# Performance work log

Hardware: AMD Instinct MI355X
Metric: run time of the kernel (lower is better)

The kernel has to match this reference:

```python
import jax, jax.numpy as jnp
import numpy as np

N_NODES = 50000
N_EDGES = 500000
N_GRAPHS = 512


def _segmean(vals, ids, num):
    # avg aggregation: segment mean with safe divide for empty segments
    s = jax.ops.segment_sum(vals, ids, num_segments=num)
    c = jax.ops.segment_sum(jnp.ones((vals.shape[0], 1), vals.dtype), ids, num_segments=num)
    return s / jnp.maximum(c, 1.0)


def setup_inputs() -> dict:
    key = jax.random.key(0)
    ks = iter(jax.random.split(key, 64))

    def nrm(shape, scale=0.05):
        return jax.random.normal(next(ks), shape, dtype=jnp.float32) * scale

    inp = {}
    inp['x'] = nrm((N_NODES, 64), 1.0)
    inp['e'] = nrm((N_EDGES, 32), 1.0)
    inp['u'] = nrm((N_GRAPHS, 64), 1.0)
    inp['a'] = nrm((N_GRAPHS, 8), 1.0)
    inp['senders'] = jax.random.randint(next(ks), (N_EDGES,), 0, N_NODES)
    inp['receivers'] = jax.random.randint(next(ks), (N_EDGES,), 0, N_NODES)
    inp['node_graph'] = jnp.sort(jax.random.randint(next(ks), (N_NODES,), 0, N_GRAPHS))
    inp['edge_graph'] = jnp.sort(jax.random.randint(next(ks), (N_EDGES,), 0, N_GRAPHS))
    # block 1 (hidden 256)
    inp['We1'] = nrm((32, 256)); inp['be1'] = jnp.zeros((256,), jnp.float32)
    inp['Wn1'] = nrm((64, 256)); inp['Win1'] = nrm((256, 256)); inp['Wout1'] = nrm((256, 256)); inp['bn1'] = jnp.zeros((256,), jnp.float32)
    inp['Wg1'] = nrm((64, 256)); inp['Wgn1'] = nrm((256, 256)); inp['Wge1'] = nrm((256, 256)); inp['bg1'] = jnp.zeros((256,), jnp.float32)
    # block 2 (hidden 128)
    inp['We2'] = nrm((256, 128)); inp['be2'] = jnp.zeros((128,), jnp.float32)
    inp['Wn2'] = nrm((256, 128)); inp['Win2'] = nrm((128, 128)); inp['Wout2'] = nrm((128, 128)); inp['bn2'] = jnp.zeros((128,), jnp.float32)
    inp['Wg2'] = nrm((256, 128)); inp['Wgn2'] = nrm((128, 128)); inp['Wge2'] = nrm((128, 128)); inp['bg2'] = jnp.zeros((128,), jnp.float32)
    # global readout (global_features only)
    inp['Wga'] = nrm((128, 128)); inp['bga'] = jnp.zeros((128,), jnp.float32)
    # action-value MLP: (128 + 8) -> 256 -> 256 -> 1
    inp['Wa1'] = nrm((136, 256)); inp['ba1'] = jnp.zeros((256,), jnp.float32)
    inp['Wa2'] = nrm((256, 256)); inp['ba2'] = jnp.zeros((256,), jnp.float32)
    inp['Wa3'] = nrm((256, 1)); inp['ba3'] = jnp.zeros((1,), jnp.float32)
    return inp


def reference(x, e, u, a, senders, receivers, node_graph, edge_graph,
              We1, be1, Wn1, Win1, Wout1, bn1, Wg1, Wgn1, Wge1, bg1,
              We2, be2, Wn2, Win2, Wout2, bn2, Wg2, Wgn2, Wge2, bg2,
              Wga, bga, Wa1, ba1, Wa2, ba2, Wa3, ba3):
    # --- GraphNetwork block 1 (hidden 256) ---
    e1 = jax.nn.relu(e @ We1 + be1)                                  # [E,256]
    inc1 = _segmean(e1, receivers, N_NODES)                          # avg incoming per node
    out1 = _segmean(e1, senders, N_NODES)                            # avg outgoing per node
    n1 = jax.nn.relu(x @ Wn1 + inc1 @ Win1 + out1 @ Wout1 + bn1)     # [N,256]
    u1 = jax.nn.relu(u @ Wg1 + _segmean(n1, node_graph, N_GRAPHS) @ Wgn1
                     + _segmean(e1, edge_graph, N_GRAPHS) @ Wge1 + bg1)  # [B,256]
    # --- GraphNetwork block 2 (hidden 128) ---
    e2 = jax.nn.relu(e1 @ We2 + be2)                                 # [E,128]
    inc2 = _segmean(e2, receivers, N_NODES)
    out2 = _segmean(e2, senders, N_NODES)
    n2 = jax.nn.relu(n1 @ Wn2 + inc2 @ Win2 + out2 @ Wout2 + bn2)    # [N,128]
    u2 = jax.nn.relu(u1 @ Wg2 + _segmean(n2, node_graph, N_GRAPHS) @ Wgn2
                     + _segmean(e2, edge_graph, N_GRAPHS) @ Wge2 + bg2)  # [B,128]
    # --- global readout + action-value MLP ---
    state_value = u2 @ Wga + bga                                     # [B,128]
    h = jnp.concatenate([state_value, a], axis=1)                    # [B,136]
    h = jax.nn.relu(h @ Wa1 + ba1)
    h = jax.nn.relu(h @ Wa2 + ba2)
    return h @ Wa3 + ba3                                             # [B,1]
```

## Files before the change

### kernel.cpp

```cpp
#include <hip/hip_runtime.h>
#include <hip/hip_bf16.h>

#define N_NODES 50000
#define N_EDGES 500000
#define N_GRAPHS 512

#define FXS16 2048.0f
#define FXI16 4.8828125e-4f

__device__ __forceinline__ unsigned long long pk16x4(float4 v) {
    const unsigned long long a = (unsigned int)fmaf(v.x, FXS16, 0.5f);
    const unsigned long long b = (unsigned int)fmaf(v.y, FXS16, 0.5f);
    const unsigned long long c = (unsigned int)fmaf(v.z, FXS16, 0.5f);
    const unsigned long long d = (unsigned int)fmaf(v.w, FXS16, 0.5f);
    return a | (b << 16) | (c << 32) | (d << 48);
}

typedef __attribute__((ext_vector_type(8))) short bf16x8;
typedef __attribute__((ext_vector_type(4))) float f32x4;

__global__ __launch_bounds__(256) void prep_kernel(
    const float* __restrict__ We2,  const float* __restrict__ Wn1,
    const float* __restrict__ Win1, const float* __restrict__ Wout1,
    const float* __restrict__ Wn2,  const float* __restrict__ Win2,
    const float* __restrict__ Wout2, const float* __restrict__ We1,
    __hip_bfloat16* __restrict__ Wt2,  __hip_bfloat16* __restrict__ Wn1t,
    __hip_bfloat16* __restrict__ Win1t,__hip_bfloat16* __restrict__ Wout1t,
    __hip_bfloat16* __restrict__ Wn2t, __hip_bfloat16* __restrict__ Win2t,
    __hip_bfloat16* __restrict__ Wout2t, __hip_bfloat16* __restrict__ We1t)
{
    const int b = blockIdx.x, t = threadIdx.x;
    const float* src; __hip_bfloat16* dst; int K, N, base;
    if (b < 128)      { src = We2;   dst = Wt2;    K = 256; N = 128; base = 0; }
    else if (b < 192) { src = Wn1;   dst = Wn1t;   K = 64;  N = 256; base = 128; }
    else if (b < 448) { src = Win1;  dst = Win1t;  K = 256; N = 256; base = 192; }
    else if (b < 704) { src = Wout1; dst = Wout1t; K = 256; N = 256; base = 448; }
    else if (b < 832) { src = Wn2;   dst = Wn2t;   K = 256; N = 128; base = 704; }
    else if (b < 896) { src = Win2;  dst = Win2t;  K = 128; N = 128; base = 832; }
    else if (b < 960) { src = Wout2; dst = Wout2t; K = 128; N = 128; base = 896; }
    else              { src = We1;   dst = We1t;   K = 32;  N = 256; base = 960; }
    const int i = (b - base) * 256 + t;
    const int n = i / K, k = i - n * K;
    dst[i] = __float2bfloat16(src[(size_t)k * N + n]);
}

__global__ __launch_bounds__(256) void convert_e_kernel(
    const float* __restrict__ e, __hip_bfloat16* __restrict__ ebf)
{
    const long i = (long)blockIdx.x * 256 + threadIdx.x;
    if (i * 8 >= (long)N_EDGES * 32) return;
    const float4 v0 = *(const float4*)&e[i * 8];
    const float4 v1 = *(const float4*)&e[i * 8 + 4];
    __hip_bfloat16* d = &ebf[i * 8];
    *(__hip_bfloat162*)&d[0] = __float22bfloat162_rn(make_float2(v0.x, v0.y));
    *(__hip_bfloat162*)&d[2] = __float22bfloat162_rn(make_float2(v0.z, v0.w));
    *(__hip_bfloat162*)&d[4] = __float22bfloat162_rn(make_float2(v1.x, v1.y));
    *(__hip_bfloat162*)&d[6] = __float22bfloat162_rn(make_float2(v1.z, v1.w));
}


#define NTILES 196

__global__ __launch_bounds__(256) void count_kernel(
    const int* __restrict__ senders, const int* __restrict__ receivers,
    unsigned int* __restrict__ rc, unsigned int* __restrict__ sc)
{
    const int i = blockIdx.x * 256 + threadIdx.x;
    if (i < N_EDGES) {
        atomicAdd(&rc[receivers[i]], 1u);
        atomicAdd(&sc[senders[i]], 1u);
    }
}

__global__ __launch_bounds__(256) void scan_tile_sum(
    const unsigned int* __restrict__ rc, const unsigned int* __restrict__ sc,
    unsigned int* __restrict__ tsR, unsigned int* __restrict__ tsS)
{
    const int b = blockIdx.x;
    const int sel = (b >= NTILES);
    const int tile = sel ? b - NTILES : b;
    const unsigned int* src = sel ? sc : rc;
    unsigned int* ts = sel ? tsS : tsR;
    const int t = threadIdx.x;
    const int i = tile * 256 + t;
    unsigned int v = (i < N_NODES) ? src[i] : 0u;
    __shared__ unsigned int s[256];
    s[t] = v; __syncthreads();
    for (int off = 128; off > 0; off >>= 1) {
        if (t < off) s[t] += s[t + off];
        __syncthreads();
    }
    if (t == 0) ts[tile] = s[0];
}

__global__ __launch_bounds__(256) void scan_tile_offsets(
    unsigned int* __restrict__ tsR, unsigned int* __restrict__ tsS,
    int* __restrict__ roff, int* __restrict__ soff)
{
    __shared__ unsigned int s[256];
    const int t = threadIdx.x;
    for (int sel = 0; sel < 2; sel++) {
        unsigned int* ts = sel ? tsS : tsR;
        int* off = sel ? soff : roff;
        unsigned int v = (t < NTILES) ? ts[t] : 0u;
        s[t] = v; __syncthreads();
        for (int o = 1; o < 256; o <<= 1) {
            unsigned int x = (t >= o) ? s[t - o] : 0u;
            __syncthreads();
            s[t] += x;
            __syncthreads();
        }
        const unsigned int incl = s[t];
        if (t < NTILES) ts[t] = incl - v;
        if (t == NTILES - 1) off[N_NODES] = (int)incl;
        __syncthreads();
    }
}

__global__ __launch_bounds__(256) void scan_finalize(
    const unsigned int* __restrict__ rc, const unsigned int* __restrict__ sc,
    const unsigned int* __restrict__ tsR, const unsigned int* __restrict__ tsS,
    int* __restrict__ roff, int* __restrict__ soff,
    unsigned int* __restrict__ wpR, unsigned int* __restrict__ wpS)
{
    const int b = blockIdx.x;
    const int sel = (b >= NTILES);
    const int tile = sel ? b - NTILES : b;
    const unsigned int* src = sel ? sc : rc;
    const unsigned int* ts = sel ? tsS : tsR;
    int* off = sel ? soff : roff;
    unsigned int* wp = sel ? wpS : wpR;
    const int t = threadIdx.x, i = tile * 256 + t;
    unsigned int v = (i < N_NODES) ? src[i] : 0u;
    __shared__ unsigned int s[256];
    s[t] = v; __syncthreads();
    for (int o = 1; o < 256; o <<= 1) {
        unsigned int x = (t >= o) ? s[t - o] : 0u;
        __syncthreads();
        s[t] += x;
        __syncthreads();
    }
    const unsigned int excl = s[t] - v + ts[tile];
    if (i < N_NODES) { off[i] = (int)excl; wp[i] = excl; }
}

__global__ __launch_bounds__(256) void csr_fill(
    const int* __restrict__ senders, const int* __restrict__ receivers,
    unsigned int* __restrict__ wpR, unsigned int* __restrict__ wpS,
    int* __restrict__ csrR, int* __restrict__ csrS)
{
    const int i = blockIdx.x * 256 + threadIdx.x;
    if (i < N_EDGES) {
        csrR[atomicAdd(&wpR[receivers[i]], 1u)] = i;
        csrS[atomicAdd(&wpS[senders[i]], 1u)] = i;
    }
}

#define EPB 32
#define EBP 40
#define E1P 264
#define E2P 132

__global__ __launch_bounds__(256) void edge_kernel_e2(
    const float* __restrict__ e,
    const int* __restrict__ edge_graph,
    const __hip_bfloat16* __restrict__ We1t, const float* __restrict__ be1,
    const __hip_bfloat16* __restrict__ Wt2,
    const float* __restrict__ be2,
    float* __restrict__ ge1, float* __restrict__ ge2, float* __restrict__ gecnt)
{
    __shared__ __hip_bfloat16 eB[EPB * EBP];
    __shared__ __hip_bfloat16 e1B[EPB * E1P];
    __shared__ float e2L[EPB * E2P];
    __shared__ int gidx[EPB];

    const int t = threadIdx.x;
    const long e0 = (long)blockIdx.x * EPB;

    {
        const int j = t >> 3, c4 = (t & 7) * 4;
        const float4 v = *(const float4*)&e[(e0 + j) * 32 + c4];
        __hip_bfloat16* d = &eB[j * EBP + c4];
        *(__hip_bfloat162*)&d[0] = __float22bfloat162_rn(make_float2(v.x, v.y));
        *(__hip_bfloat162*)&d[2] = __float22bfloat162_rn(make_float2(v.z, v.w));
    }
    if (t < EPB) gidx[t] = edge_graph[e0 + t];
    __syncthreads();

    const int wv = t >> 6, ln = t & 63;
    const int r0 = ln & 15, q = ln >> 4;

    #pragma unroll
    for (int mt = 0; mt < 2; mt++) {
        const bf16x8 a = *(const bf16x8*)&eB[(mt * 16 + r0) * EBP + q * 8];
        #pragma unroll
        for (int nn = 0; nn < 4; nn++) {
            const int n = (wv * 4 + nn) * 16 + r0;
            const bf16x8 wb = *(const bf16x8*)&We1t[(size_t)n * 32 + q * 8];
            f32x4 c = {0.f, 0.f, 0.f, 0.f};
            c = __builtin_amdgcn_mfma_f32_16x16x32_bf16(a, wb, c, 0, 0, 0);
            const float bz = be1[n];
            #pragma unroll
            for (int r = 0; r < 4; r++)
                e1B[(mt * 16 + q * 4 + r) * E1P + n] =
                    __float2bfloat16(fmaxf(c[r] + bz, 0.f));
        }
    }
    __syncthreads();

    {
        f32x4 acc[2][2] = {{{0.f,0.f,0.f,0.f},{0.f,0.f,0.f,0.f}},
                           {{0.f,0.f,0.f,0.f},{0.f,0.f,0.f,0.f}}};
        const int n0 = (2 * wv) * 16 + r0;
        const int n1 = (2 * wv + 1) * 16 + r0;
        #pragma unroll
        for (int kb = 0; kb < 8; kb++) {
            const int k0 = kb * 32 + q * 8;
            const bf16x8 a0 = *(const bf16x8*)&e1B[(r0) * E1P + k0];
            const bf16x8 a1 = *(const bf16x8*)&e1B[(16 + r0) * E1P + k0];
            const bf16x8 b0 = *(const bf16x8*)&Wt2[(size_t)n0 * 256 + k0];
            const bf16x8 b1 = *(const bf16x8*)&Wt2[(size_t)n1 * 256 + k0];
            acc[0][0] = __builtin_amdgcn_mfma_f32_16x16x32_bf16(a0, b0, acc[0][0], 0, 0, 0);
            acc[0][1] = __builtin_amdgcn_mfma_f32_16x16x32_bf16(a0, b1, acc[0][1], 0, 0, 0);
            acc[1][0] = __builtin_amdgcn_mfma_f32_16x16x32_bf16(a1, b0, acc[1][0], 0, 0, 0);
            acc[1][1] = __builtin_amdgcn_mfma_f32_16x16x32_bf16(a1, b1, acc[1][1], 0, 0, 0);
        }
        const float bz0 = be2[2 * wv * 16 + r0];
        const float bz1 = be2[(2 * wv + 1) * 16 + r0];
        #pragma unroll
        for (int mt = 0; mt < 2; mt++) {
            const int m = mt * 16 + q * 4;
            #pragma unroll
            for (int r = 0; r < 4; r++) {
                e2L[(m + r) * E2P + 2 * wv * 16 + r0]       = fmaxf(acc[mt][0][r] + bz0, 0.f);
                e2L[(m + r) * E2P + (2 * wv + 1) * 16 + r0] = fmaxf(acc[mt][1][r] + bz1, 0.f);
            }
        }
    }
    __syncthreads();

    if (gidx[0] == gidx[EPB - 1]) {
        const int g = gidx[0];
        float s = 0.f;
        #pragma unroll
        for (int j = 0; j < EPB; j++) s += __bfloat162float(e1B[j * E1P + t]);
        atomicAdd(&ge1[(size_t)g * 256 + t], s);
        if (t < 128) {
            float s2 = 0.f;
            #pragma unroll
            for (int j = 0; j < EPB; j++) s2 += e2L[j * E2P + t];
            atomicAdd(&ge2[(size_t)g * 128 + t], s2);
        }
        if (t == 0) atomicAdd(&gecnt[g], (float)EPB);
    } else {
        int j = 0;
        while (j < EPB) {
            const int g = gidx[j];
            int j2 = j;
            float s = 0.f;
            while (j2 < EPB && gidx[j2] == g) { s += __bfloat162float(e1B[j2 * E1P + t]); j2++; }
            atomicAdd(&ge1[(size_t)g * 256 + t], s);
            if (t < 128) {
                float s2 = 0.f;
                for (int jj = j; jj < j2; jj++) s2 += e2L[jj * E2P + t];
                atomicAdd(&ge2[(size_t)g * 128 + t], s2);
            }
            if (t == 0) atomicAdd(&gecnt[g], (float)(j2 - j));
            j = j2;
        }
    }
}

#define ANPB 16
#define CHK 64
#define ESP 40
#define E1CP 312
#define E2CP 184
#define JADDR(j, c, P) ((j) * (P) + (c) + ((((j) >> 3) & 3) << 4))

__global__ __launch_bounds__(256) void agg_kernel(
    const __hip_bfloat16* __restrict__ ebf,
    const int* __restrict__ roff, const int* __restrict__ soff,
    const int* __restrict__ csrR, const int* __restrict__ csrS,
    const __hip_bfloat16* __restrict__ We1t, const float* __restrict__ be1,
    const __hip_bfloat16* __restrict__ Wt2, const float* __restrict__ be2,
    __hip_bfloat16* __restrict__ i1d, __hip_bfloat16* __restrict__ o1d,
    __hip_bfloat16* __restrict__ i2d, __hip_bfloat16* __restrict__ o2d)
{
    __shared__ __hip_bfloat16 eS[2][CHK * ESP];
    __shared__ __hip_bfloat16 e1C[CHK * E1CP];
    __shared__ __hip_bfloat16 e2C[CHK * E2CP];
    __shared__ int idL[2][CHK];
    __shared__ int segL[2][CHK];
    __shared__ int offL[ANPB + 1];

    const int t = threadIdx.x;
    int b = blockIdx.x;
    const int side = (b >= (N_NODES / ANPB));
    if (side) b -= N_NODES / ANPB;
    const int n0 = b * ANPB;
    const int* off = side ? soff : roff;
    const int* lst = side ? csrS : csrR;
    __hip_bfloat16* d1 = side ? o1d : i1d;
    __hip_bfloat16* d2 = side ? o2d : i2d;

    if (t <= ANPB) offL[t] = off[n0 + t];
    __syncthreads();
    const int base = offL[0], end = offL[ANPB];
    const int nchunks = (end - base + CHK - 1) / CHK;

    const int wv = t >> 6, ln = t & 63;
    const int r0 = ln & 15, q = ln >> 4;
    const int srow = t >> 2, scol = (t & 3) * 8;

    f32x4 s1[4] = {{0.f,0.f,0.f,0.f},{0.f,0.f,0.f,0.f},
                   {0.f,0.f,0.f,0.f},{0.f,0.f,0.f,0.f}};
    f32x4 s2[2] = {{0.f,0.f,0.f,0.f},{0.f,0.f,0.f,0.f}};

    float bz1[4], bz2[2];
    #pragma unroll
    for (int nn = 0; nn < 4; nn++) bz1[nn] = be1[(wv * 4 + nn) * 16 + r0];
    #pragma unroll
    for (int nn = 0; nn < 2; nn++) bz2[nn] = be2[(wv * 2 + nn) * 16 + r0];

    if (t < CHK) {
        const int p = base + t;
        int sg = -1, id = 0;
        if (p < end) {
            id = lst[p];
            sg = 0;
            #pragma unroll
            for (int j = 1; j < ANPB; j++) sg += (p >= offL[j]) ? 1 : 0;
        }
        idL[0][t] = id; segL[0][t] = sg;
    }
    __syncthreads();
    {
        bf16x8 v = {0, 0, 0, 0, 0, 0, 0, 0};
        if (segL[0][srow] >= 0) v = *(const bf16x8*)&ebf[(size_t)idL[0][srow] * 32 + scol];
        *(bf16x8*)&eS[0][srow * ESP + scol] = v;
    }
    __syncthreads();

    int cur = 0;
    for (int c = 0; c < nchunks; c++) {
        const int nxt = cur ^ 1;

        int idn = 0, sgn = -1;
        if (t < CHK) {
            const int p = base + (c + 1) * CHK + t;
            if (c + 1 < nchunks && p < end) {
                idn = lst[p];
                sgn = 0;
                #pragma unroll
                for (int j = 1; j < ANPB; j++) sgn += (p >= offL[j]) ? 1 : 0;
            }
        }

        bf16x8 ind[2];
        #pragma unroll
        for (int ks = 0; ks < 2; ks++)
            #pragma unroll
            for (int i = 0; i < 8; i++)
                ind[ks][i] = (segL[cur][ks * 32 + q * 8 + i] == r0) ? (short)0x3F80 : (short)0;

        #pragma unroll
        for (int mt = 0; mt < 4; mt++) {
            const bf16x8 a = *(const bf16x8*)&eS[cur][(mt * 16 + r0) * ESP + q * 8];
            #pragma unroll
            for (int nn = 0; nn < 4; nn++) {
                const int n = (wv * 4 + nn) * 16 + r0;
                const bf16x8 wb = *(const bf16x8*)&We1t[(size_t)n * 32 + q * 8];
                f32x4 cc = {0.f, 0.f, 0.f, 0.f};
                cc = __builtin_amdgcn_mfma_f32_16x16x32_bf16(a, wb, cc, 0, 0, 0);
                #pragma unroll
                for (int r = 0; r < 4; r++)
                    e1C[JADDR(mt * 16 + q * 4 + r, n, E1CP)] =
                        __float2bfloat16(fmaxf(cc[r] + bz1[nn], 0.f));
            }
        }
        if (t < CHK) { idL[nxt][t] = idn; segL[nxt][t] = sgn; }
        __syncthreads();

        bf16x8 pre = {0, 0, 0, 0, 0, 0, 0, 0};
        if (segL[nxt][srow] >= 0)
            pre = *(const bf16x8*)&ebf[(size_t)idL[nxt][srow] * 32 + scol];

        #pragma unroll
        for (int ks = 0; ks < 2; ks++) {
            #pragma unroll
            for (int nn = 0; nn < 4; nn++) {
                const int n = (wv * 4 + nn) * 16 + r0;
                bf16x8 bfr;
                #pragma unroll
                for (int i = 0; i < 8; i++)
                    bfr[i] = *(const short*)&e1C[JADDR(ks * 32 + q * 8 + i, n, E1CP)];
                s1[nn] = __builtin_amdgcn_mfma_f32_16x16x32_bf16(ind[ks], bfr, s1[nn], 0, 0, 0);
            }
        }

        #pragma unroll
        for (int mt = 0; mt < 4; mt++) {
            f32x4 cc[2] = {{0.f,0.f,0.f,0.f},{0.f,0.f,0.f,0.f}};
            #pragma unroll
            for (int ks = 0; ks < 8; ks++) {
                const bf16x8 a = *(const bf16x8*)&e1C[JADDR(mt * 16 + r0, ks * 32 + q * 8, E1CP)];
                #pragma unroll
                for (int nn = 0; nn < 2; nn++) {
                    const int n = (wv * 2 + nn) * 16 + r0;
                    const bf16x8 wb = *(const bf16x8*)&Wt2[(size_t)n * 256 + ks * 32 + q * 8];
                    cc[nn] = __builtin_amdgcn_mfma_f32_16x16x32_bf16(a, wb, cc[nn], 0, 0, 0);
                }
            }
            #pragma unroll
            for (int nn = 0; nn < 2; nn++) {
                const int n = (wv * 2 + nn) * 16 + r0;
                #pragma unroll
                for (int r = 0; r < 4; r++)
                    e2C[JADDR(mt * 16 + q * 4 + r, n, E2CP)] =
                        __float2bfloat16(fmaxf(cc[nn][r] + bz2[nn], 0.f));
            }
        }
        __syncthreads();

        #pragma unroll
        for (int ks = 0; ks < 2; ks++) {
            #pragma unroll
            for (int nn = 0; nn < 2; nn++) {
                const int n = (wv * 2 + nn) * 16 + r0;
                bf16x8 bfr;
                #pragma unroll
                for (int i = 0; i < 8; i++)
                    bfr[i] = *(const short*)&e2C[JADDR(ks * 32 + q * 8 + i, n, E2CP)];
                s2[nn] = __builtin_amdgcn_mfma_f32_16x16x32_bf16(ind[ks], bfr, s2[nn], 0, 0, 0);
            }
        }

        *(bf16x8*)&eS[nxt][srow * ESP + scol] = pre;
        __syncthreads();
        cur = nxt;
    }

    {
        float inv[4];
        #pragma unroll
        for (int r = 0; r < 4; r++) {
            const int m = q * 4 + r;
            const int deg = offL[m + 1] - offL[m];
            inv[r] = 1.f / (float)(deg > 0 ? deg : 1);
        }
        #pragma unroll
        for (int nn = 0; nn < 4; nn++) {
            const int n = (wv * 4 + nn) * 16 + r0;
            #pragma unroll
            for (int r = 0; r < 4; r++)
                e1C[(q * 4 + r) * E1CP + n] = __float2bfloat16(s1[nn][r] * inv[r]);
        }
        #pragma unroll
        for (int nn = 0; nn < 2; nn++) {
            const int n = (wv * 2 + nn) * 16 + r0;
            #pragma unroll
            for (int r = 0; r < 4; r++)
                e2C[(q * 4 + r) * E2CP + n] = __float2bfloat16(s2[nn][r] * inv[r]);
        }
    }
    __syncthreads();
    for (int i = t; i < ANPB * 32; i += 256) {
        const int j = i >> 5, c8 = (i & 31) * 8;
        *(bf16x8*)&d1[(size_t)(n0 + j) * 256 + c8] = *(const bf16x8*)&e1C[j * E1CP + c8];
    }
    for (int i = t; i < ANPB * 16; i += 256) {
        const int j = i >> 4, c8 = (i & 15) * 8;
        *(bf16x8*)&d2[(size_t)(n0 + j) * 128 + c8] = *(const bf16x8*)&e2C[j * E2CP + c8];
    }
}

#define NPB 16
#define XP  72
#define K1P 264
#define K2P 136

__global__ __launch_bounds__(256) void node_kernel_dense(
    const float* __restrict__ x,
    const int* __restrict__ node_graph,
    const __hip_bfloat16* __restrict__ i1d, const __hip_bfloat16* __restrict__ o1d,
    const __hip_bfloat16* __restrict__ i2d, const __hip_bfloat16* __restrict__ o2d,
    const __hip_bfloat16* __restrict__ Wn1t, const __hip_bfloat16* __restrict__ Win1t,
    const __hip_bfloat16* __restrict__ Wout1t, const float* __restrict__ bn1,
    const __hip_bfloat16* __restrict__ Wn2t, const __hip_bfloat16* __restrict__ Win2t,
    const __hip_bfloat16* __restrict__ Wout2t, const float* __restrict__ bn2,
    float* __restrict__ gn1, float* __restrict__ gn2, float* __restrict__ gncnt)
{
    __shared__ __hip_bfloat16 xB[NPB * XP];
    __shared__ __hip_bfloat16 i1B[NPB * K1P];
    __shared__ __hip_bfloat16 o1B[NPB * K1P];
    __shared__ __hip_bfloat16 i2B[NPB * K2P];
    __shared__ __hip_bfloat16 o2B[NPB * K2P];
    __shared__ __hip_bfloat16 n1B[NPB * K1P];
    __shared__ __hip_bfloat16 n2B[NPB * K2P];
    __shared__ int gI[NPB];

    const int t = threadIdx.x;
    const long n0 = (long)blockIdx.x * NPB;

    if (t < NPB) gI[t] = node_graph[n0 + t];
    for (int i = t; i < NPB * 16; i += 256) {
        const int j = i >> 4, c4 = (i & 15) * 4;
        const float4 v = *(const float4*)&x[(n0 + j) * 64 + c4];
        *(__hip_bfloat162*)&xB[j * XP + c4]     = __float22bfloat162_rn(make_float2(v.x, v.y));
        *(__hip_bfloat162*)&xB[j * XP + c4 + 2] = __float22bfloat162_rn(make_float2(v.z, v.w));
    }
    for (int i = t; i < NPB * 32; i += 256) {
        const int j = i >> 5, c8 = (i & 31) * 8;
        *(bf16x8*)&i1B[j * K1P + c8] = *(const bf16x8*)&i1d[(size_t)(n0 + j) * 256 + c8];
        *(bf16x8*)&o1B[j * K1P + c8] = *(const bf16x8*)&o1d[(size_t)(n0 + j) * 256 + c8];
    }
    for (int i = t; i < NPB * 16; i += 256) {
        const int j = i >> 4, c8 = (i & 15) * 8;
        *(bf16x8*)&i2B[j * K2P + c8] = *(const bf16x8*)&i2d[(size_t)(n0 + j) * 128 + c8];
        *(bf16x8*)&o2B[j * K2P + c8] = *(const bf16x8*)&o2d[(size_t)(n0 + j) * 128 + c8];
    }
    __syncthreads();

    const int wv = t >> 6, ln = t & 63;
    const int r0 = ln & 15, q = ln >> 4;

    {
        f32x4 acc[4] = {{0.f,0.f,0.f,0.f},{0.f,0.f,0.f,0.f},
                        {0.f,0.f,0.f,0.f},{0.f,0.f,0.f,0.f}};
        #pragma unroll
        for (int ks = 0; ks < 2; ks++) {
            const int k0 = ks * 32 + q * 8;
            const bf16x8 a = *(const bf16x8*)&xB[r0 * XP + k0];
            #pragma unroll
            for (int nn = 0; nn < 4; nn++) {
                const int n = (wv * 4 + nn) * 16 + r0;
                const bf16x8 b = *(const bf16x8*)&Wn1t[(size_t)n * 64 + k0];
                acc[nn] = __builtin_amdgcn_mfma_f32_16x16x32_bf16(a, b, acc[nn], 0, 0, 0);
            }
        }
        #pragma unroll
        for (int ks = 0; ks < 8; ks++) {
            const int k0 = ks * 32 + q * 8;
            const bf16x8 a = *(const bf16x8*)&i1B[r0 * K1P + k0];
            #pragma unroll
            for (int nn = 0; nn < 4; nn++) {
                const int n = (wv * 4 + nn) * 16 + r0;
                const bf16x8 b = *(const bf16x8*)&Win1t[(size_t)n * 256 + k0];
                acc[nn] = __builtin_amdgcn_mfma_f32_16x16x32_bf16(a, b, acc[nn], 0, 0, 0);
            }
        }
        #pragma unroll
        for (int ks = 0; ks < 8; ks++) {
            const int k0 = ks * 32 + q * 8;
            const bf16x8 a = *(const bf16x8*)&o1B[r0 * K1P + k0];
            #pragma unroll
            for (int nn = 0; nn < 4; nn++) {
                const int n = (wv * 4 + nn) * 16 + r0;
                const bf16x8 b = *(const bf16x8*)&Wout1t[(size_t)n * 256 + k0];
                acc[nn] = __builtin_amdgcn_mfma_f32_16x16x32_bf16(a, b, acc[nn], 0, 0, 0);
            }
        }
        #pragma unroll
        for (int nn = 0; nn < 4; nn++) {
            const int n = (wv * 4 + nn) * 16 + r0;
            const float bz = bn1[n];
            #pragma unroll
            for (int r = 0; r < 4; r++) {
                const int m = q * 4 + r;
                n1B[m * K1P + n] = __float2bfloat16(fmaxf(acc[nn][r] + bz, 0.f));
            }
        }
    }
    __syncthreads();

    if (gI[0] == gI[NPB - 1]) {
        float s = 0.f;
        #pragma unroll
        for (int j = 0; j < NPB; j++) s += __bfloat162float(n1B[j * K1P + t]);
        atomicAdd(&gn1[(size_t)gI[0] * 256 + t], s);
        if (t == 0) atomicAdd(&gncnt[gI[0]], (float)NPB);
// ... 314 lines not shown
        atomicAdd(&rcnt[ridx[t]], 1.f);
        atomicAdd(&scnt[sidx[t]], 1.f);
    }
}

__global__ __launch_bounds__(256) void node_kernel(
    const float* __restrict__ x,
    const int* __restrict__ node_graph,
    const unsigned long long* __restrict__ inc1u, const unsigned long long* __restrict__ out1u,
    const unsigned long long* __restrict__ inc2u, const unsigned long long* __restrict__ out2u,
    const float* __restrict__ rcnt, const float* __restrict__ scnt,
    const __hip_bfloat16* __restrict__ Wn1t, const __hip_bfloat16* __restrict__ Win1t,
    const __hip_bfloat16* __restrict__ Wout1t, const float* __restrict__ bn1,
    const __hip_bfloat16* __restrict__ Wn2t, const __hip_bfloat16* __restrict__ Win2t,
    const __hip_bfloat16* __restrict__ Wout2t, const float* __restrict__ bn2,
    float* __restrict__ gn1, float* __restrict__ gn2, float* __restrict__ gncnt)
{
    __shared__ __hip_bfloat16 xB[NPB * XP];
    __shared__ __hip_bfloat16 i1B[NPB * K1P];
    __shared__ __hip_bfloat16 o1B[NPB * K1P];
    __shared__ __hip_bfloat16 i2B[NPB * K2P];
    __shared__ __hip_bfloat16 o2B[NPB * K2P];
    __shared__ __hip_bfloat16 n1B[NPB * K1P];
    __shared__ __hip_bfloat16 n2B[NPB * K2P];
    __shared__ int gI[NPB];
    __shared__ float rrcp[NPB], srcp[NPB];

    const int t = threadIdx.x;
    const long n0 = (long)blockIdx.x * NPB;

    if (t < NPB) {
        gI[t] = node_graph[n0 + t];
        rrcp[t] = FXI16 / fmaxf(rcnt[n0 + t], 1.f);
        srcp[t] = FXI16 / fmaxf(scnt[n0 + t], 1.f);
    }
    for (int i = t; i < NPB * 16; i += 256) {
        const int j = i >> 4, c4 = (i & 15) * 4;
        const float4 v = *(const float4*)&x[(n0 + j) * 64 + c4];
        *(__hip_bfloat162*)&xB[j * XP + c4]     = __float22bfloat162_rn(make_float2(v.x, v.y));
        *(__hip_bfloat162*)&xB[j * XP + c4 + 2] = __float22bfloat162_rn(make_float2(v.z, v.w));
    }
    __syncthreads();

    for (int i = t; i < NPB * 64; i += 256) {
        const int j = i >> 6, w = i & 63;
        const size_t n = (size_t)(n0 + j);
        const unsigned long long av = inc1u[n * 64 + w];
        const unsigned long long bv = out1u[n * 64 + w];
        const float rr = rrcp[j], sr = srcp[j];
        const float2 a01 = make_float2((float)(unsigned int)(av & 0xFFFF) * rr,
                                       (float)(unsigned int)((av >> 16) & 0xFFFF) * rr);
        const float2 a23 = make_float2((float)(unsigned int)((av >> 32) & 0xFFFF) * rr,
                                       (float)(unsigned int)(av >> 48) * rr);
        const float2 b01 = make_float2((float)(unsigned int)(bv & 0xFFFF) * sr,
                                       (float)(unsigned int)((bv >> 16) & 0xFFFF) * sr);
        const float2 b23 = make_float2((float)(unsigned int)((bv >> 32) & 0xFFFF) * sr,
                                       (float)(unsigned int)(bv >> 48) * sr);
        *(__hip_bfloat162*)&i1B[j * K1P + 4 * w]     = __float22bfloat162_rn(a01);
        *(__hip_bfloat162*)&i1B[j * K1P + 4 * w + 2] = __float22bfloat162_rn(a23);
        *(__hip_bfloat162*)&o1B[j * K1P + 4 * w]     = __float22bfloat162_rn(b01);
        *(__hip_bfloat162*)&o1B[j * K1P + 4 * w + 2] = __float22bfloat162_rn(b23);
    }
    for (int i = t; i < NPB * 32; i += 256) {
        const int j = i >> 5, w = i & 31;
        const size_t n = (size_t)(n0 + j);
        const unsigned long long av = inc2u[n * 32 + w];
        const unsigned long long bv = out2u[n * 32 + w];
        const float rr = rrcp[j], sr = srcp[j];
        const float2 a01 = make_float2((float)(unsigned int)(av & 0xFFFF) * rr,
                                       (float)(unsigned int)((av >> 16) & 0xFFFF) * rr);
        const float2 a23 = make_float2((float)(unsigned int)((av >> 32) & 0xFFFF) * rr,
                                       (float)(unsigned int)(av >> 48) * rr);
        const float2 b01 = make_float2((float)(unsigned int)(bv & 0xFFFF) * sr,
                                       (float)(unsigned int)((bv >> 16) & 0xFFFF) * sr);
        const float2 b23 = make_float2((float)(unsigned int)((bv >> 32) & 0xFFFF) * sr,
                                       (float)(unsigned int)(bv >> 48) * sr);
        *(__hip_bfloat162*)&i2B[j * K2P + 4 * w]     = __float22bfloat162_rn(a01);
        *(__hip_bfloat162*)&i2B[j * K2P + 4 * w + 2] = __float22bfloat162_rn(a23);
        *(__hip_bfloat162*)&o2B[j * K2P + 4 * w]     = __float22bfloat162_rn(b01);
        *(__hip_bfloat162*)&o2B[j * K2P + 4 * w + 2] = __float22bfloat162_rn(b23);
    }
    __syncthreads();

    const int wv = t >> 6, ln = t & 63;
    const int r0 = ln & 15, q = ln >> 4;

    {
        f32x4 acc[4] = {{0.f,0.f,0.f,0.f},{0.f,0.f,0.f,0.f},
                        {0.f,0.f,0.f,0.f},{0.f,0.f,0.f,0.f}};
        #pragma unroll
        for (int ks = 0; ks < 2; ks++) {
            const int k0 = ks * 32 + q * 8;
            const bf16x8 a = *(const bf16x8*)&xB[r0 * XP + k0];
            #pragma unroll
            for (int nn = 0; nn < 4; nn++) {
                const int n = (wv * 4 + nn) * 16 + r0;
                const bf16x8 b = *(const bf16x8*)&Wn1t[(size_t)n * 64 + k0];
                acc[nn] = __builtin_amdgcn_mfma_f32_16x16x32_bf16(a, b, acc[nn], 0, 0, 0);
            }
        }
        #pragma unroll
        for (int ks = 0; ks < 8; ks++) {
            const int k0 = ks * 32 + q * 8;
            const bf16x8 a = *(const bf16x8*)&i1B[r0 * K1P + k0];
            #pragma unroll
            for (int nn = 0; nn < 4; nn++) {
                const int n = (wv * 4 + nn) * 16 + r0;
                const bf16x8 b = *(const bf16x8*)&Win1t[(size_t)n * 256 + k0];
                acc[nn] = __builtin_amdgcn_mfma_f32_16x16x32_bf16(a, b, acc[nn], 0, 0, 0);
            }
        }
        #pragma unroll
        for (int ks = 0; ks < 8; ks++) {
            const int k0 = ks * 32 + q * 8;
            const bf16x8 a = *(const bf16x8*)&o1B[r0 * K1P + k0];
            #pragma unroll
            for (int nn = 0; nn < 4; nn++) {
                const int n = (wv * 4 + nn) * 16 + r0;
                const bf16x8 b = *(const bf16x8*)&Wout1t[(size_t)n * 256 + k0];
                acc[nn] = __builtin_amdgcn_mfma_f32_16x16x32_bf16(a, b, acc[nn], 0, 0, 0);
            }
        }
        #pragma unroll
        for (int nn = 0; nn < 4; nn++) {
            const int n = (wv * 4 + nn) * 16 + r0;
            const float bz = bn1[n];
            #pragma unroll
            for (int r = 0; r < 4; r++) {
                const int m = q * 4 + r;
                n1B[m * K1P + n] = __float2bfloat16(fmaxf(acc[nn][r] + bz, 0.f));
            }
        }
    }
    __syncthreads();

    if (gI[0] == gI[NPB - 1]) {
        float s = 0.f;
        #pragma unroll
        for (int j = 0; j < NPB; j++) s += __bfloat162float(n1B[j * K1P + t]);
        atomicAdd(&gn1[(size_t)gI[0] * 256 + t], s);
        if (t == 0) atomicAdd(&gncnt[gI[0]], (float)NPB);
    } else {
        int j = 0;
        while (j < NPB) {
            const int g = gI[j];
            int j2 = j;
            float s = 0.f;
            while (j2 < NPB && gI[j2] == g) { s += __bfloat162float(n1B[j2 * K1P + t]); j2++; }
            atomicAdd(&gn1[(size_t)g * 256 + t], s);
            if (t == 0) atomicAdd(&gncnt[g], (float)(j2 - j));
            j = j2;
        }
    }

    {
        f32x4 acc[2] = {{0.f,0.f,0.f,0.f},{0.f,0.f,0.f,0.f}};
        #pragma unroll
        for (int ks = 0; ks < 8; ks++) {
            const int k0 = ks * 32 + q * 8;
            const bf16x8 a = *(const bf16x8*)&n1B[r0 * K1P + k0];
            #pragma unroll
            for (int nn = 0; nn < 2; nn++) {
                const int n = (wv * 2 + nn) * 16 + r0;
                const bf16x8 b = *(const bf16x8*)&Wn2t[(size_t)n * 256 + k0];
                acc[nn] = __builtin_amdgcn_mfma_f32_16x16x32_bf16(a, b, acc[nn], 0, 0, 0);
            }
        }
        #pragma unroll
        for (int ks = 0; ks < 4; ks++) {
            const int k0 = ks * 32 + q * 8;
            const bf16x8 a = *(const bf16x8*)&i2B[r0 * K2P + k0];
            #pragma unroll
            for (int nn = 0; nn < 2; nn++) {
                const int n = (wv * 2 + nn) * 16 + r0;
                const bf16x8 b = *(const bf16x8*)&Win2t[(size_t)n * 128 + k0];
                acc[nn] = __builtin_amdgcn_mfma_f32_16x16x32_bf16(a, b, acc[nn], 0, 0, 0);
            }
        }
        #pragma unroll
        for (int ks = 0; ks < 4; ks++) {
            const int k0 = ks * 32 + q * 8;
            const bf16x8 a = *(const bf16x8*)&o2B[r0 * K2P + k0];
            #pragma unroll
            for (int nn = 0; nn < 2; nn++) {
                const int n = (wv * 2 + nn) * 16 + r0;
                const bf16x8 b = *(const bf16x8*)&Wout2t[(size_t)n * 128 + k0];
                acc[nn] = __builtin_amdgcn_mfma_f32_16x16x32_bf16(a, b, acc[nn], 0, 0, 0);
            }
        }
        #pragma unroll
        for (int nn = 0; nn < 2; nn++) {
            const int n = (wv * 2 + nn) * 16 + r0;
            const float bz = bn2[n];
            #pragma unroll
            for (int r = 0; r < 4; r++) {
                const int m = q * 4 + r;
                n2B[m * K2P + n] = __float2bfloat16(fmaxf(acc[nn][r] + bz, 0.f));
            }
        }
    }
    __syncthreads();

    if (t < 128) {
        if (gI[0] == gI[NPB - 1]) {
            float s = 0.f;
            #pragma unroll
            for (int j = 0; j < NPB; j++) s += __bfloat162float(n2B[j * K2P + t]);
            atomicAdd(&gn2[(size_t)gI[0] * 128 + t], s);
        } else {
            int j = 0;
            while (j < NPB) {
                const int g = gI[j];
                int j2 = j;
                float s = 0.f;
                while (j2 < NPB && gI[j2] == g) { s += __bfloat162float(n2B[j2 * K2P + t]); j2++; }
                atomicAdd(&gn2[(size_t)g * 128 + t], s);
                j = j2;
            }
        }
    }
}

extern "C" void kernel_launch(void* const* d_in, const int* in_sizes, int n_in,
                              void* d_out, int out_size, void* d_ws, size_t ws_size,
                              hipStream_t stream) {
    const float* x          = (const float*)d_in[0];
    const float* e          = (const float*)d_in[1];
    const float* u          = (const float*)d_in[2];
    const float* a          = (const float*)d_in[3];
    const int*   senders    = (const int*)d_in[4];
    const int*   receivers  = (const int*)d_in[5];
    const int*   node_graph = (const int*)d_in[6];
    const int*   edge_graph = (const int*)d_in[7];
    const float* We1 = (const float*)d_in[8];  const float* be1 = (const float*)d_in[9];
    const float* Wn1 = (const float*)d_in[10]; const float* Win1 = (const float*)d_in[11];
    const float* Wout1 = (const float*)d_in[12]; const float* bn1 = (const float*)d_in[13];
    const float* Wg1 = (const float*)d_in[14]; const float* Wgn1 = (const float*)d_in[15];
    const float* Wge1 = (const float*)d_in[16]; const float* bg1 = (const float*)d_in[17];
    const float* We2 = (const float*)d_in[18]; const float* be2 = (const float*)d_in[19];
    const float* Wn2 = (const float*)d_in[20]; const float* Win2 = (const float*)d_in[21];
    const float* Wout2 = (const float*)d_in[22]; const float* bn2 = (const float*)d_in[23];
    const float* Wg2 = (const float*)d_in[24]; const float* Wgn2 = (const float*)d_in[25];
    const float* Wge2 = (const float*)d_in[26]; const float* bg2 = (const float*)d_in[27];
    const float* Wga = (const float*)d_in[28]; const float* bga = (const float*)d_in[29];
    const float* Wa1 = (const float*)d_in[30]; const float* ba1 = (const float*)d_in[31];
    const float* Wa2 = (const float*)d_in[32]; const float* ba2 = (const float*)d_in[33];
    const float* Wa3 = (const float*)d_in[34]; const float* ba3 = (const float*)d_in[35];

    {
        char* p = (char*)d_ws;
        auto take = [&p](size_t bytes) {
            char* q = p; p += (bytes + 15) & ~(size_t)15; return q;
        };
        unsigned int* rcntU = (unsigned int*)take((size_t)N_NODES * 4);
        unsigned int* scntU = (unsigned int*)take((size_t)N_NODES * 4);
        float* ge1   = (float*)take((size_t)N_GRAPHS * 256 * 4);
        float* ge2   = (float*)take((size_t)N_GRAPHS * 128 * 4);
        float* gecnt = (float*)take((size_t)N_GRAPHS * 4);
        float* gn1   = (float*)take((size_t)N_GRAPHS * 256 * 4);
        float* gn2   = (float*)take((size_t)N_GRAPHS * 128 * 4);
        float* gncnt = (float*)take((size_t)N_GRAPHS * 4);
        const size_t zero_bytes = (size_t)(p - (char*)d_ws);
        int* roff = (int*)take((size_t)(N_NODES + 1) * 4);
        int* soff = (int*)take((size_t)(N_NODES + 1) * 4);
        unsigned int* wpR = (unsigned int*)take((size_t)N_NODES * 4);
        unsigned int* wpS = (unsigned int*)take((size_t)N_NODES * 4);
        unsigned int* tsR = (unsigned int*)take(256 * 4);
        unsigned int* tsS = (unsigned int*)take(256 * 4);
        int* csrR = (int*)take((size_t)N_EDGES * 4);
        int* csrS = (int*)take((size_t)N_EDGES * 4);
        __hip_bfloat16* ebf = (__hip_bfloat16*)take((size_t)N_EDGES * 32 * 2);
        __hip_bfloat16* i1d = (__hip_bfloat16*)take((size_t)N_NODES * 256 * 2);
        __hip_bfloat16* o1d = (__hip_bfloat16*)take((size_t)N_NODES * 256 * 2);
        __hip_bfloat16* i2d = (__hip_bfloat16*)take((size_t)N_NODES * 128 * 2);
        __hip_bfloat16* o2d = (__hip_bfloat16*)take((size_t)N_NODES * 128 * 2);
        __hip_bfloat16* Wt2    = (__hip_bfloat16*)take((size_t)128 * 256 * 2);
        __hip_bfloat16* Wn1t   = (__hip_bfloat16*)take((size_t)256 * 64 * 2);
        __hip_bfloat16* Win1t  = (__hip_bfloat16*)take((size_t)256 * 256 * 2);
        __hip_bfloat16* Wout1t = (__hip_bfloat16*)take((size_t)256 * 256 * 2);
        __hip_bfloat16* Wn2t   = (__hip_bfloat16*)take((size_t)128 * 256 * 2);
        __hip_bfloat16* Win2t  = (__hip_bfloat16*)take((size_t)128 * 128 * 2);
        __hip_bfloat16* Wout2t = (__hip_bfloat16*)take((size_t)128 * 128 * 2);
        __hip_bfloat16* We1t   = (__hip_bfloat16*)take((size_t)256 * 32 * 2);
        const size_t needed = (size_t)(p - (char*)d_ws);

        if (ws_size >= needed) {
            hipMemsetAsync(d_ws, 0, zero_bytes, stream);

            prep_kernel<<<992, 256, 0, stream>>>(
                We2, Wn1, Win1, Wout1, Wn2, Win2, Wout2, We1,
                Wt2, Wn1t, Win1t, Wout1t, Wn2t, Win2t, Wout2t, We1t);

            convert_e_kernel<<<(N_EDGES * 32 / 8 + 255) / 256, 256, 0, stream>>>(e, ebf);

            count_kernel<<<(N_EDGES + 255) / 256, 256, 0, stream>>>(
                senders, receivers, rcntU, scntU);
            scan_tile_sum<<<2 * NTILES, 256, 0, stream>>>(rcntU, scntU, tsR, tsS);
            scan_tile_offsets<<<1, 256, 0, stream>>>(tsR, tsS, roff, soff);
            scan_finalize<<<2 * NTILES, 256, 0, stream>>>(
                rcntU, scntU, tsR, tsS, roff, soff, wpR, wpS);
            csr_fill<<<(N_EDGES + 255) / 256, 256, 0, stream>>>(
                senders, receivers, wpR, wpS, csrR, csrS);

            edge_kernel_e2<<<N_EDGES / EPB, 256, 0, stream>>>(
                e, edge_graph, We1t, be1, Wt2, be2, ge1, ge2, gecnt);

            agg_kernel<<<2 * (N_NODES / ANPB), 256, 0, stream>>>(
                ebf, roff, soff, csrR, csrS, We1t, be1, Wt2, be2,
                i1d, o1d, i2d, o2d);

            node_kernel_dense<<<N_NODES / NPB, 256, 0, stream>>>(
                x, node_graph, i1d, o1d, i2d, o2d,
                Wn1t, Win1t, Wout1t, bn1, Wn2t, Win2t, Wout2t, bn2,
                gn1, gn2, gncnt);

            graph_kernel<<<N_GRAPHS, 256, 0, stream>>>(
                u, a, ge1, ge2, gecnt, gn1, gn2, gncnt,
                Wg1, Wgn1, Wge1, bg1, Wg2, Wgn2, Wge2, bg2,
                Wga, bga, Wa1, ba1, Wa2, ba2, Wa3, ba3, (float*)d_out);
            return;
        }
    }

    unsigned long long* uw = (unsigned long long*)d_ws;
    unsigned long long* inc1u = uw;                       uw += (size_t)N_NODES * 64;
    unsigned long long* out1u = uw;                       uw += (size_t)N_NODES * 64;
    unsigned long long* inc2u = uw;                       uw += (size_t)N_NODES * 32;
    unsigned long long* out2u = uw;                       uw += (size_t)N_NODES * 32;
    float* fw = (float*)uw;
    float* rcnt = fw;  fw += N_NODES;
    float* scnt = fw;  fw += N_NODES;
    float* ge1  = fw;  fw += (size_t)N_GRAPHS * 256;
    float* ge2  = fw;  fw += (size_t)N_GRAPHS * 128;
    float* gecnt = fw; fw += N_GRAPHS;
    float* gn1  = fw;  fw += (size_t)N_GRAPHS * 256;
    float* gn2  = fw;  fw += (size_t)N_GRAPHS * 128;
    float* gncnt = fw; fw += N_GRAPHS;
    const size_t total_bytes = (char*)fw - (char*)d_ws;
    __hip_bfloat16* bw = (__hip_bfloat16*)fw;
    __hip_bfloat16* Wt2    = bw;  bw += 128 * 256;
    __hip_bfloat16* Wn1t   = bw;  bw += 256 * 64;
    __hip_bfloat16* Win1t  = bw;  bw += 256 * 256;
    __hip_bfloat16* Wout1t = bw;  bw += 256 * 256;
    __hip_bfloat16* Wn2t   = bw;  bw += 128 * 256;
    __hip_bfloat16* Win2t  = bw;  bw += 128 * 128;
    __hip_bfloat16* Wout2t = bw;  bw += 128 * 128;
    __hip_bfloat16* We1t   = bw;  bw += 256 * 32;

    hipMemsetAsync(d_ws, 0, total_bytes, stream);

    prep_kernel<<<992, 256, 0, stream>>>(
        We2, Wn1, Win1, Wout1, Wn2, Win2, Wout2, We1,
        Wt2, Wn1t, Win1t, Wout1t, Wn2t, Win2t, Wout2t, We1t);

    edge_kernel<<<N_EDGES / EPB, 256, 0, stream>>>(
        e, senders, receivers, edge_graph, We1, be1, Wt2, be2,
        inc1u, out1u, inc2u, out2u, rcnt, scnt, ge1, ge2, gecnt);

    node_kernel<<<N_NODES / NPB, 256, 0, stream>>>(
        x, node_graph, inc1u, out1u, inc2u, out2u, rcnt, scnt,
        Wn1t, Win1t, Wout1t, bn1, Wn2t, Win2t, Wout2t, bn2, gn1, gn2, gncnt);

    graph_kernel<<<N_GRAPHS, 256, 0, stream>>>(
        u, a, ge1, ge2, gecnt, gn1, gn2, gncnt,
        Wg1, Wgn1, Wge1, bg1, Wg2, Wgn2, Wge2, bg2,
        Wga, bga, Wa1, ba1, Wa2, ba2, Wa3, ba3, (float*)d_out);
}
```

Measured before the change: 902.8 us.

## Retile edge kernel to 64 edges per block with register-held per-graph reductions

The edge-level kernel that produces per-graph edge sums now handles 64 edges per block instead of 32 and uses a swizzled LDS layout for the e1 tile. The e2 results are kept in registers rather than written to LDS. Per-graph sums are formed in registers with masked accumulation and cross-lane shuffles before the atomics, which removes the e2 LDS buffer and the serial per-thread column loops. The trade-off is higher register pressure (launch bounds set to 2 blocks) and a masked reduction that loops once per graph segment in each tile.

```diff
diff --git a/kernel.cpp b/kernel.cpp
--- a/kernel.cpp
+++ b/kernel.cpp
@@ -18,6 +18,15 @@
 
 typedef __attribute__((ext_vector_type(8))) short bf16x8;
 typedef __attribute__((ext_vector_type(4))) float f32x4;
+
+#define ESP 40
+#define E1CP 312
+#define E2CP 184
+#define JADDR(j, c, P) ((j) * (P) + (c) + ((((j) >> 3) & 3) << 4))
+
+#define EPB 32
+#define E1P 264
+#define E2P 132
 
 __global__ __launch_bounds__(256) void prep_kernel(
     const float* __restrict__ We2,  const float* __restrict__ Wn1,
@@ -156,12 +165,9 @@
     }
 }
 
-#define EPB 32
-#define EBP 40
-#define E1P 264
-#define E2P 132
-
-__global__ __launch_bounds__(256) void edge_kernel_e2(
+#define EPB2 64
+
+__global__ __launch_bounds__(256, 2) void edge_kernel_e2(
     const float* __restrict__ e,
     const int* __restrict__ edge_graph,
     const __hip_bfloat16* __restrict__ We1t, const float* __restrict__ be1,
@@ -169,114 +175,127 @@
     const float* __restrict__ be2,
     float* __restrict__ ge1, float* __restrict__ ge2, float* __restrict__ gecnt)
 {
-    __shared__ __hip_bfloat16 eB[EPB * EBP];
-    __shared__ __hip_bfloat16 e1B[EPB * E1P];
-    __shared__ float e2L[EPB * E2P];
-    __shared__ int gidx[EPB];
+    __shared__ __hip_bfloat16 eS[EPB2 * ESP];
+    __shared__ __hip_bfloat16 e1C[EPB2 * E1CP];
+    __shared__ int gidx[EPB2];
 
     const int t = threadIdx.x;
-    const long e0 = (long)blockIdx.x * EPB;
-
-    {
-        const int j = t >> 3, c4 = (t & 7) * 4;
-        const float4 v = *(const float4*)&e[(e0 + j) * 32 + c4];
-        __hip_bfloat16* d = &eB[j * EBP + c4];
-        *(__hip_bfloat162*)&d[0] = __float22bfloat162_rn(make_float2(v.x, v.y));
-        *(__hip_bfloat162*)&d[2] = __float22bfloat162_rn(make_float2(v.z, v.w));
-    }
-    if (t < EPB) gidx[t] = edge_graph[e0 + t];
+    const long e0 = (long)blockIdx.x * EPB2;
+    const int cnt = (int)((N_EDGES - e0 < EPB2) ? (N_EDGES - e0) : EPB2);
+
+    {
+        const int srow = t >> 2, scol = (t & 3) * 8;
+        __hip_bfloat16 tmp[8];
+        #pragma unroll
+        for (int i = 0; i < 8; i++) tmp[i] = __float2bfloat16(0.f);
+        if (srow < cnt) {
+            const float4 a0 = *(const float4*)&e[(e0 + srow) * 32 + scol];
+            const float4 a1 = *(const float4*)&e[(e0 + srow) * 32 + scol + 4];
+            *(__hip_bfloat162*)&tmp[0] = __float22bfloat162_rn(make_float2(a0.x, a0.y));
+            *(__hip_bfloat162*)&tmp[2] = __float22bfloat162_rn(make_float2(a0.z, a0.w));
+            *(__hip_bfloat162*)&tmp[4] = __float22bfloat162_rn(make_float2(a1.x, a1.y));
+            *(__hip_bfloat162*)&tmp[6] = __float22bfloat162_rn(make_float2(a1.z, a1.w));
+        }
+        *(bf16x8*)&eS[srow * ESP + scol] = *(bf16x8*)tmp;
+    }
+    if (t < EPB2) gidx[t] = (t < cnt) ? edge_graph[e0 + t] : -1;
     __syncthreads();
 
     const int wv = t >> 6, ln = t & 63;
     const int r0 = ln & 15, q = ln >> 4;
 
+    float bz1[4], bz2[2];
     #pragma unroll
-    for (int mt = 0; mt < 2; mt++) {
-        const bf16x8 a = *(const bf16x8*)&eB[(mt * 16 + r0) * EBP + q * 8];
+    for (int nn = 0; nn < 4; nn++) bz1[nn] = be1[(wv * 4 + nn) * 16 + r0];
+    #pragma unroll
+    for (int nn = 0; nn < 2; nn++) bz2[nn] = be2[(wv * 2 + nn) * 16 + r0];
+
+    float ev1[4][4][4];
+    #pragma unroll
+    for (int mt = 0; mt < 4; mt++) {
+        const bf16x8 a = *(const bf16x8*)&eS[(mt * 16 + r0) * ESP + q * 8];
         #pragma unroll
         for (int nn = 0; nn < 4; nn++) {
             const int n = (wv * 4 + nn) * 16 + r0;
             const bf16x8 wb = *(const bf16x8*)&We1t[(size_t)n * 32 + q * 8];
             f32x4 c = {0.f, 0.f, 0.f, 0.f};
             c = __builtin_amdgcn_mfma_f32_16x16x32_bf16(a, wb, c, 0, 0, 0);
-            const float bz = be1[n];
+            #pragma unroll
+            for (int r = 0; r < 4; r++) {
+                const float v = fmaxf(c[r] + bz1[nn], 0.f);
+                ev1[mt][nn][r] = v;
+                e1C[JADDR(mt * 16 + q * 4 + r, n, E1CP)] = __float2bfloat16(v);
+            }
+        }
+    }
+    __syncthreads();
+
+    float ev2[4][2][4];
+    #pragma unroll
+    for (int mt = 0; mt < 4; mt++) {
+        f32x4 c[2] = {{0.f,0.f,0.f,0.f},{0.f,0.f,0.f,0.f}};
+        #pragma unroll
+        for (int ks = 0; ks < 8; ks++) {
+            const bf16x8 a = *(const bf16x8*)&e1C[JADDR(mt * 16 + r0, ks * 32 + q * 8, E1CP)];
+            #pragma unroll
+            for (int nn = 0; nn < 2; nn++) {
+                const int n = (wv * 2 + nn) * 16 + r0;
+                const bf16x8 wb = *(const bf16x8*)&Wt2[(size_t)n * 256 + ks * 32 + q * 8];
+                c[nn] = __builtin_amdgcn_mfma_f32_16x16x32_bf16(a, wb, c[nn], 0, 0, 0);
+            }
+        }
+        #pragma unroll
+        for (int nn = 0; nn < 2; nn++)
             #pragma unroll
             for (int r = 0; r < 4; r++)
-                e1B[(mt * 16 + q * 4 + r) * E1P + n] =
-                    __float2bfloat16(fmaxf(c[r] + bz, 0.f));
-        }
-    }
-    __syncthreads();
-
-    {
-        f32x4 acc[2][2] = {{{0.f,0.f,0.f,0.f},{0.f,0.f,0.f,0.f}},
-                           {{0.f,0.f,0.f,0.f},{0.f,0.f,0.f,0.f}}};
-        const int n0 = (2 * wv) * 16 + r0;
-        const int n1 = (2 * wv + 1) * 16 + r0;
-        #pragma unroll
-        for (int kb = 0; kb < 8; kb++) {
-            const int k0 = kb * 32 + q * 8;
-            const bf16x8 a0 = *(const bf16x8*)&e1B[(r0) * E1P + k0];
-            const bf16x8 a1 = *(const bf16x8*)&e1B[(16 + r0) * E1P + k0];
-            const bf16x8 b0 = *(const bf16x8*)&Wt2[(size_t)n0 * 256 + k0];
-            const bf16x8 b1 = *(const bf16x8*)&Wt2[(size_t)n1 * 256 + k0];
-            acc[0][0] = __builtin_amdgcn_mfma_f32_16x16x32_bf16(a0, b0, acc[0][0], 0, 0, 0);
-            acc[0][1] = __builtin_amdgcn_mfma_f32_16x16x32_bf16(a0, b1, acc[0][1], 0, 0, 0);
-            acc[1][0] = __builtin_amdgcn_mfma_f32_16x16x32_bf16(a1, b0, acc[1][0], 0, 0, 0);
-            acc[1][1] = __builtin_amdgcn_mfma_f32_16x16x32_bf16(a1, b1, acc[1][1], 0, 0, 0);
-        }
-        const float bz0 = be2[2 * wv * 16 + r0];
-        const float bz1 = be2[(2 * wv + 1) * 16 + r0];
-        #pragma unroll
-        for (int mt = 0; mt < 2; mt++) {
-            const int m = mt * 16 + q * 4;
-            #pragma unroll
-            for (int r = 0; r < 4; r++) {
-                e2L[(m + r) * E2P + 2 * wv * 16 + r0]       = fmaxf(acc[mt][0][r] + bz0, 0.f);
-                e2L[(m + r) * E2P + (2 * wv + 1) * 16 + r0] = fmaxf(acc[mt][1][r] + bz1, 0.f);
-            }
-        }
-    }
-    __syncthreads();
-
-    if (gidx[0] == gidx[EPB - 1]) {
-        const int g = gidx[0];
-        float s = 0.f;
-        #pragma unroll
-        for (int j = 0; j < EPB; j++) s += __bfloat162float(e1B[j * E1P + t]);
-        atomicAdd(&ge1[(size_t)g * 256 + t], s);
-        if (t < 128) {
-            float s2 = 0.f;
-            #pragma unroll
-            for (int j = 0; j < EPB; j++) s2 += e2L[j * E2P + t];
-            atomicAdd(&ge2[(size_t)g * 128 + t], s2);
-        }
-        if (t == 0) atomicAdd(&gecnt[g], (float)EPB);
-    } else {
-        int j = 0;
-        while (j < EPB) {
-            const int g = gidx[j];
-            int j2 = j;
-            float s = 0.f;
-            while (j2 < EPB && gidx[j2] == g) { s += __bfloat162float(e1B[j2 * E1P + t]); j2++; }
-            atomicAdd(&ge1[(size_t)g * 256 + t], s);
-            if (t < 128) {
-                float s2 = 0.f;
-                for (int jj = j; jj < j2; jj++) s2 += e2L[jj * E2P + t];
-                atomicAdd(&ge2[(size_t)g * 128 + t], s2);
-            }
-            if (t == 0) atomicAdd(&gecnt[g], (float)(j2 - j));
-            j = j2;
-        }
+                ev2[mt][nn][r] = fmaxf(c[nn][r] + bz2[nn], 0.f);
+    }
+
+    int j = 0;
+    while (j < cnt) {
+        const int g = gidx[j];
+        int j2 = j + 1;
+        while (j2 < cnt && gidx[j2] == g) j2++;
+        #pragma unroll
+        for (int nn = 0; nn < 4; nn++) {
+            float ps = 0.f;
+            #pragma unroll
+            for (int mt = 0; mt < 4; mt++)
+                #pragma unroll
+                for (int r = 0; r < 4; r++) {
+                    const int m = mt * 16 + q * 4 + r;
+                    ps += (m >= j && m < j2) ? ev1[mt][nn][r] : 0.f;
+                }
+            ps += __shfl_xor(ps, 16, 64);
+            ps += __shfl_xor(ps, 32, 64);
+            if (q == 0) atomicAdd(&ge1[(size_t)g * 256 + (wv * 4 + nn) * 16 + r0], ps);
+        }
+        #pragma unroll
+        for (int nn = 0; nn < 2; nn++) {
+            float ps = 0.f;
+            #pragma unroll
+            for (int mt = 0; mt < 4; mt++)
+                #pragma unroll
+                for (int r = 0; r < 4; r++) {
+                    const int m = mt * 16 + q * 4 + r;
+                    ps += (m >= j && m < j2) ? ev2[mt][nn][r] : 0.f;
+                }
+            ps += __shfl_xor(ps, 16, 64);
+            ps += __shfl_xor(ps, 32, 64);
+            if (q == 0) atomicAdd(&ge2[(size_t)g * 128 + (wv * 2 + nn) * 16 + r0], ps);
+        }
+        j = j2;
+    }
+
+    if (t < cnt && (t == 0 || gidx[t] != gidx[t - 1])) {
+        int j2 = t + 1;
+        while (j2 < cnt && gidx[j2] == gidx[t]) j2++;
+        atomicAdd(&gecnt[gidx[t]], (float)(j2 - t));
     }
 }
 
 #define ANPB 16
 #define CHK 64
-#define ESP 40
-#define E1CP 312
-#define E2CP 184
-#define JADDR(j, c, P) ((j) * (P) + (c) + ((((j) >> 3) & 3) << 4))
 
 __global__ __launch_bounds__(256) void agg_kernel(
     const __hip_bfloat16* __restrict__ ebf,
@@ -1197,7 +1216,7 @@
             csr_fill<<<(N_EDGES + 255) / 256, 256, 0, stream>>>(
                 senders, receivers, wpR, wpS, csrR, csrS);
 
-            edge_kernel_e2<<<N_EDGES / EPB, 256, 0, stream>>>(
+            edge_kernel_e2<<<(N_EDGES + EPB2 - 1) / EPB2, 256, 0, stream>>>(
                 e, edge_graph, We1t, be1, Wt2, be2, ge1, ge2, gecnt);
 
             agg_kernel<<<2 * (N_NODES / ANPB), 256, 0, stream>>>(
```

New measurement: 989.6 us. 9.6% more time.
